# Optimization experiments

Hardware: AMD Instinct MI355X
Metric: run time of the kernel (lower is better)

## Reference

```python
import jax, jax.numpy as jnp
import numpy as np

H = 1024   # hidden_size
V = 1024   # output_size
B = 64     # batch
L = 512    # seq_len


def setup_inputs() -> dict:
    key = jax.random.key(0)
    ks = jax.random.split(key, 14)
    n = jax.random.normal
    s = jnp.float32(0.02)
    return {
        "encoder_output": n(ks[0], (L, B, H), jnp.float32),
        "hidden": n(ks[1], (B, H), jnp.float32),
        "decoder_output": n(ks[2], (B, H), jnp.float32),
        "Wa": n(ks[3], (H, 2 * H), jnp.float32) * s,
        "ba": n(ks[4], (H,), jnp.float32) * s,
        "v": n(ks[5], (H,), jnp.float32) * s,
        "W_ih": n(ks[6], (3 * H, 2 * H), jnp.float32) * s,
        "b_ih": n(ks[7], (3 * H,), jnp.float32) * s,
        "W_hh": n(ks[8], (3 * H, H), jnp.float32) * s,
        "b_hh": n(ks[9], (3 * H,), jnp.float32) * s,
        "Wo": n(ks[10], (H, 3 * H), jnp.float32) * s,
        "bo": n(ks[11], (H,), jnp.float32) * s,
        "Wf": n(ks[12], (V, H), jnp.float32) * s,
        "bf": n(ks[13], (V,), jnp.float32) * s,
    }


def reference(encoder_output, hidden, decoder_output, Wa, ba, v,
              W_ih, b_ih, W_hh, b_hh, Wo, bo, Wf, bf):
    Lx, Bx, Hx = encoder_output.shape
    # energy[b,l] = v . (Wa @ cat(hidden[b], enc[l,b]) + ba)
    # split Wa into hidden-part and encoder-part; fold v into each (linearity)
    Wa_h, Wa_e = Wa[:, :Hx], Wa[:, Hx:]
    vh = Wa_h.T @ v            # (H,)
    ve = Wa_e.T @ v            # (H,)
    vb = ba @ v                # scalar
    # encoder contribution to energies is constant across decode steps
    enc_score = jnp.einsum('lbh,h->bl', encoder_output, ve)  # (B, L)

    def gru_cell(x, h):
        # torch.nn.GRUCell math, gate order [r, z, n]
        gi = x @ W_ih.T + b_ih
        gh = h @ W_hh.T + b_hh
        i_r, i_z, i_n = jnp.split(gi, 3, axis=1)
        h_r, h_z, h_n = jnp.split(gh, 3, axis=1)
        r = jax.nn.sigmoid(i_r + h_r)
        z = jax.nn.sigmoid(i_z + h_z)
        n_g = jnp.tanh(i_n + r * h_n)
        return (1.0 - z) * n_g + z * h

    def step(carry, _):
        h, dec = carry
        energy = (h @ vh + vb)[:, None] + enc_score          # (B, L)
        a = jax.nn.softmax(energy, axis=1)                   # softmax over seq
        ctx = jnp.einsum('bl,lbh->bh', a, encoder_output)    # (B, H)
        h_new = gru_cell(jnp.concatenate([dec, ctx], axis=1), h)
        dec_new = jax.nn.softmax(
            jnp.concatenate([h_new, dec, ctx], axis=1) @ Wo.T + bo, axis=1)
        out = jax.nn.softmax(dec_new @ Wf.T + bf, axis=1)    # (B, V)
        return (h_new, dec_new), out

    _, outs = jax.lax.scan(step, (hidden, decoder_output), None, length=Lx)
    return outs  # (L, B, V)
```

## Files before the change

### kernel.cpp

```cpp
#include <hip/hip_runtime.h>
#include <hip/hip_bf16.h>


#define HH 1024
#define BB 64
#define LL 512
#define VV 1024

typedef short bf16x8 __attribute__((ext_vector_type(8)));
typedef float f32x4 __attribute__((ext_vector_type(4)));

__device__ __forceinline__ short f2bf(float x) {
  union { float f; unsigned u; } a; a.f = x;
  unsigned r = (a.u + 0x7FFF + ((a.u >> 16) & 1)) >> 16;
  return (short)r;
}

__device__ __forceinline__ float fsig(float x) {
  return 1.0f / (1.0f + __expf(-x));
}
__device__ __forceinline__ float ftanh(float x) {
  float ex = __expf(2.0f * x);
  return 1.0f - 2.0f / (ex + 1.0f);
}

__device__ __forceinline__ unsigned long long ld64c(const void* p) {
  return __hip_atomic_load((const unsigned long long*)p, __ATOMIC_RELAXED, __HIP_MEMORY_SCOPE_AGENT);
}
__device__ __forceinline__ unsigned ld32c(const void* p) {
  return __hip_atomic_load((const unsigned*)p, __ATOMIC_RELAXED, __HIP_MEMORY_SCOPE_AGENT);
}
__device__ __forceinline__ void st32c(void* p, unsigned v) {
  __hip_atomic_store((unsigned*)p, v, __ATOMIC_RELAXED, __HIP_MEMORY_SCOPE_AGENT);
}
__device__ __forceinline__ void stfc(float* p, float v) {
  union { float f; unsigned u; } a; a.f = v;
  st32c(p, a.u);
}

static constexpr size_t OFF_VE    = 0;
static constexpr size_t OFF_ES    = 4096;
static constexpr size_t OFF_A     = OFF_ES    + 131072;
static constexpr size_t OFF_CTX   = OFF_A     + 131072;
static constexpr size_t OFF_GICTX = OFF_CTX   + 262144;
static constexpr size_t OFF_OC    = OFF_GICTX + 786432;
static constexpr size_t OFF_FLAGS = OFF_OC    + 262144;
static constexpr size_t OFF_PSUMB = OFF_FLAGS + 32768;
static constexpr size_t OFF_PSUMO = OFF_PSUMB + 16384;
static constexpr size_t OFF_E2    = OFF_PSUMO + 16384;
static constexpr size_t OFF_HB0   = OFF_E2    + 131072;
static constexpr size_t OFF_HB1   = OFF_HB0   + 131072;
static constexpr size_t OFF_PACKW = OFF_HB1   + 131072;


__global__ void K_init(const float* __restrict__ hidden, const float* __restrict__ dec0,
                       short* __restrict__ hb, short* __restrict__ e2,
                       unsigned* __restrict__ flags) {
  int tid = blockIdx.x * 256 + threadIdx.x;
  if (tid < BB * HH) {
    hb[tid] = f2bf(hidden[tid]);
    e2[tid] = f2bf(dec0[tid]);
  }
  if (tid < 8192) flags[tid] = 0u;
}

__global__ void K_ve(const float* __restrict__ Wa, const float* __restrict__ v, float* __restrict__ ve) {
  int i = blockIdx.x * 64 + threadIdx.x;
  float acc = 0.f;
  for (int k = 0; k < HH; ++k) acc += Wa[(size_t)k * 2048 + 1024 + i] * v[k];
  ve[i] = acc;
}

__global__ void K_escore(const float* __restrict__ enc, const float* __restrict__ ve, float* __restrict__ es) {
  int bid = blockIdx.x;
  int lane = threadIdx.x;
  const float* row = enc + (size_t)bid * HH;
  float acc = 0.f;
  #pragma unroll
  for (int i = 0; i < 16; ++i) { int k = lane + 64 * i; acc += row[k] * ve[k]; }
  for (int m = 1; m < 64; m <<= 1) acc += __shfl_xor(acc, m);
  if (lane == 0) { int l = bid >> 6, b = bid & 63; es[b * LL + l] = acc; }
}

__global__ void K_asm(const float* __restrict__ es, float* __restrict__ a) {
  __shared__ float red[256];
  int b = blockIdx.x, tid = threadIdx.x;
  float e0 = es[b * LL + tid], e1 = es[b * LL + 256 + tid];
  red[tid] = fmaxf(e0, e1);
  __syncthreads();
  for (int s = 128; s > 0; s >>= 1) { if (tid < s) red[tid] = fmaxf(red[tid], red[tid + s]); __syncthreads(); }
  float M = red[0];
  __syncthreads();
  float x0 = expf(e0 - M), x1 = expf(e1 - M);
  red[tid] = x0 + x1;
  __syncthreads();
  for (int s = 128; s > 0; s >>= 1) { if (tid < s) red[tid] += red[tid + s]; __syncthreads(); }
  float S = red[0];
  a[b * LL + tid] = x0 / S;
  a[b * LL + 256 + tid] = x1 / S;
}

__global__ void K_ctx(const float* __restrict__ enc, const float* __restrict__ a, float* __restrict__ ctx) {
  int b = blockIdx.x >> 3, hc = blockIdx.x & 7;
  int h = hc * 128 + threadIdx.x;
  float acc = 0.f;
  for (int l = 0; l < LL; ++l) acc += a[b * LL + l] * enc[(size_t)(l * BB + b) * HH + h];
  ctx[b * HH + h] = acc;
}

__global__ void K_gictx(const float* __restrict__ ctx, const float* __restrict__ W_ih, const float* __restrict__ b_ih,
                        const float* __restrict__ Wo, const float* __restrict__ bo,
                        float* __restrict__ gictx, float* __restrict__ oc) {
  int c = blockIdx.x;
  int b = threadIdx.x;
  float acc = 0.f;
  if (c < 3072) {
    for (int k = 0; k < HH; ++k) acc += ctx[b * HH + k] * W_ih[(size_t)c * 2048 + 1024 + k];
    gictx[b * 3072 + c] = acc + b_ih[c];
  } else {
    int c2 = c - 3072;
    for (int k = 0; k < HH; ++k) acc += ctx[b * HH + k] * Wo[(size_t)c2 * 3072 + 2048 + k];
    oc[b * HH + c2] = acc + bo[c2];
  }
}

__global__ void K_pack(const float* __restrict__ W_ih, const float* __restrict__ W_hh,
                       const float* __restrict__ Wo, const float* __restrict__ Wf, short* __restrict__ packW) {
  int tid = blockIdx.x * 64 + threadIdx.x;
  int lane = tid & 63;
  int ks = (tid >> 6) & 31;
  int tile = (tid >> 11) % 9;
  int cg = tid / (9 * 32 * 64);
  int n = lane & 15;
  int k0 = ks * 32 + (lane >> 4) * 8;
  int row = cg * 16 + n;
  const float* src;
  size_t base;
  switch (tile) {
    case 0: base = (size_t)row * 2048;               src = W_ih; break;
    case 1: base = (size_t)(1024 + row) * 2048;      src = W_ih; break;
    case 2: base = (size_t)(2048 + row) * 2048;      src = W_ih; break;
    case 3: base = (size_t)row * 3072 + 1024;        src = Wo;   break;
    case 4: base = (size_t)row * 1024;               src = W_hh; break;
    case 5: base = (size_t)(1024 + row) * 1024;      src = W_hh; break;
    case 6: base = (size_t)(2048 + row) * 1024;      src = W_hh; break;
    case 7: base = (size_t)row * 1024;               src = Wf;   break;
    default: base = (size_t)row * 3072;              src = Wo;   break;
  }
  bf16x8 vv;
  #pragma unroll
  for (int j = 0; j < 8; ++j) vv[j] = f2bf(src[base + k0 + j]);
  ((bf16x8*)packW)[tid] = vv;
}


#define STAGE_SLICE(dst, srcbase)                                              \
  do {                                                                         \
    unsigned long long tv_[16];                                                \
    _Pragma("unroll")                                                          \
    for (int i_ = 0; i_ < 8; ++i_) {                                           \
      int off_ = (wave << 12) + (i_ << 9) + (lane << 3);                       \
      tv_[2 * i_]     = ld64c((srcbase) + off_);                               \
      tv_[2 * i_ + 1] = ld64c((srcbase) + off_ + 4);                           \
    }                                                                          \
    _Pragma("unroll")                                                          \
    for (int i_ = 0; i_ < 8; ++i_) {                                           \
      int off_ = (wave << 12) + (i_ << 9) + (lane << 3);                       \
      int r_ = off_ >> 10;                                                     \
      int bc_ = (off_ & 1023) << 1;                                            \
      int sw_ = bc_ ^ ((r_ & 7) << 4);                                         \
      union { unsigned long long u[2]; bf16x8 v; } x_;                         \
      x_.u[0] = tv_[2 * i_]; x_.u[1] = tv_[2 * i_ + 1];                        \
      *(bf16x8*)&(dst)[(r_ << 10) + (sw_ >> 1)] = x_.v;                        \
    }                                                                          \
  } while (0)

#define LFRAG(buf, ks) \
  (*(const bf16x8*)&(buf)[((llo) << 10) + (((((ks) * 64) + (lhi << 4)) ^ ((llo & 7) << 4)) >> 1)])

__global__ __launch_bounds__(256, 1) void K_step(
    const bf16x8* __restrict__ packW,
    short* __restrict__ e2, short* __restrict__ hb,
    const float* __restrict__ hidden,
    float* __restrict__ psumB, float* __restrict__ psumO,
    const float* __restrict__ gictx, const float* __restrict__ ocbuf,
    const float* __restrict__ b_hh, const float* __restrict__ bfv,
    float* __restrict__ outp, unsigned* __restrict__ flags) {
  const int wg = blockIdx.x;
  const int rg = wg & 3;
  const int cg = wg >> 2;
  const int tid = threadIdx.x;
  const int wave = tid >> 6;
  const int lane = tid & 63;
  const int lhi = lane >> 4;
  const int llo = lane & 15;

  __shared__ short se2[16 * 1024];
  __shared__ short sh[16 * 1024];
  __shared__ float lds_g[6][16][17];
  __shared__ float lds_p[5][16][17];
  __shared__ float lds_rs[16];

  const int wbase = cg * (9 * 32 * 64) + lane;
  const int t0 = wave * 2, t1 = wave * 2 + 1;

  bf16x8 wA0[32], wA1[32], wB8[8];
  #pragma unroll
  for (int ks = 0; ks < 32; ++ks) {
    wA0[ks] = packW[wbase + (t0 * 32 + ks) * 64];
    wA1[ks] = packW[wbase + (t1 * 32 + ks) * 64];
  }
  #pragma unroll
  for (int i = 0; i < 8; ++i) wB8[i] = packW[wbase + (8 * 32 + wave * 8 + i) * 64];
  #pragma unroll
  for (int ks = 0; ks < 32; ++ks) {
    asm volatile("" : "+v"(wA0[ks]));
    asm volatile("" : "+v"(wA1[ks]));
  }
  #pragma unroll
  for (int i = 0; i < 8; ++i) asm volatile("" : "+v"(wB8[i]));

  const int row = tid >> 4, col = tid & 15;
  const int b_ = rg * 16 + row, j = cg * 16 + col;
  const float c_gr  = gictx[b_ * 3072 + j]        + b_hh[j];
  const float c_gz  = gictx[b_ * 3072 + 1024 + j] + b_hh[1024 + j];
  const float c_gn  = gictx[b_ * 3072 + 2048 + j];
  const float c_ghn = b_hh[2048 + j];
  const float c_oc  = ocbuf[b_ * HH + j];
  float h_reg = hidden[b_ * HH + j];
  const float c_bf  = bfv[cg * 16 + llo];

  unsigned* myflags = flags + rg * (64 * 32);
  const short* e2slice = e2 + rg * 16384;
  short*       hslice  = hb + rg * 16384;

  STAGE_SLICE(sh, hslice);

  for (int t = 0; t <= LL; ++t) {
    unsigned long long pc[8];
    if (wave == 0 && t >= 1) {
      const float* pp = psumB + rg * 1024 + llo * 64 + lhi * 16;
      #pragma unroll
      for (int i = 0; i < 8; ++i) pc[i] = ld64c(pp + i * 2);
    }
    STAGE_SLICE(se2, e2slice);
    __syncthreads();

    if (wave == 0) {
      float total = 1.0f;
      if (t >= 1) {
        float s = 0.f;
        #pragma unroll
        for (int i = 0; i < 8; ++i) {
          union { unsigned long long u; float f[2]; } c; c.u = pc[i];
          s += c.f[0] + c.f[1];
        }
        s += __shfl_xor(s, 16);
        s += __shfl_xor(s, 32);
        total = s;
      }
      if (lane < 16) lds_rs[lane] = 1.0f / total;
    }

    const short* A0 = (wave < 2) ? se2 : sh;
    f32x4 acc0 = {0.f, 0.f, 0.f, 0.f}, acc1 = {0.f, 0.f, 0.f, 0.f};
    #pragma unroll
    for (int ks = 0; ks < 32; ++ks) {
      bf16x8 af0 = LFRAG(A0, ks);
      bf16x8 af1 = (wave == 3) ? LFRAG(se2, ks) : af0;
      acc0 = __builtin_amdgcn_mfma_f32_16x16x32_bf16(af0, wA0[ks], acc0, 0, 0, 0);
      acc1 = __builtin_amdgcn_mfma_f32_16x16x32_bf16(af1, wA1[ks], acc1, 0, 0, 0);
    }

    f32x4 savedA2;
    if (wave == 0) {
      #pragma unroll
      for (int r = 0; r < 4; ++r) { lds_g[0][lhi*4+r][llo] = acc0[r]; lds_g[1][lhi*4+r][llo] = acc1[r]; }
    } else if (wave == 1) {
      #pragma unroll
      for (int r = 0; r < 4; ++r) { lds_g[2][lhi*4+r][llo] = acc0[r]; savedA2[r] = acc1[r]; }
    } else if (wave == 2) {
      #pragma unroll
      for (int r = 0; r < 4; ++r) { lds_g[3][lhi*4+r][llo] = acc0[r]; lds_g[4][lhi*4+r][llo] = acc1[r]; }
    } else {
      #pragma unroll
      for (int r = 0; r < 4; ++r) lds_g[5][lhi*4+r][llo] = acc0[r];
    }
    __syncthreads();

    f32x4 eo = {0.f, 0.f, 0.f, 0.f};
    if (wave == 3 && t >= 1) {
      #pragma unroll
      for (int r = 0; r < 4; ++r) eo[r] = __expf(acc1[r] * lds_rs[lhi*4+r] + c_bf);
      #pragma unroll
      for (int r = 0; r < 4; ++r) {
        float v_ = eo[r];
        v_ += __shfl_xor(v_, 1, 16); v_ += __shfl_xor(v_, 2, 16);
        v_ += __shfl_xor(v_, 4, 16); v_ += __shfl_xor(v_, 8, 16);
        if (llo == 0) stfc(psumO + rg * 1024 + (lhi*4+r) * 64 + cg, v_);
      }
    }

    {
      float rsr = lds_rs[row];
      float gr  = lds_g[0][row][col] * rsr + lds_g[3][row][col] + c_gr;
      float gz  = lds_g[1][row][col] * rsr + lds_g[4][row][col] + c_gz;
      float gin = lds_g[2][row][col] * rsr + c_gn;
      float ghn = lds_g[5][row][col] + c_ghn;
      float rr = fsig(gr);
      float zz = fsig(gz);
      float nn = ftanh(gin + rr * ghn);
      float hnew = (1.0f - zz) * nn + zz * h_reg;
      h_reg = hnew;
      unsigned short hv = (unsigned short)f2bf(hnew);
      int other = __shfl_xor((int)hv, 1);
      if ((col & 1) == 0) {
        unsigned pk = (unsigned)hv | ((unsigned)(unsigned short)other << 16);
        st32c(hb + b_ * HH + (j & ~1), pk);
      }
    }

    {
      unsigned ep = 2u * (unsigned)t + 1u;
      __syncthreads();
      if (tid == 0) st32c(myflags + cg * 32, ep);
      if (wave == 0) {
        unsigned f;
        do { f = ld32c(myflags + lane * 32); } while (__any(f < ep));
      }
      __syncthreads();
    }

    if (t < LL) {
      STAGE_SLICE(sh, hslice);
      __syncthreads();
      f32x4 accB = {0.f, 0.f, 0.f, 0.f};
      #pragma unroll
      for (int i = 0; i < 8; ++i) {
        int ks = wave * 8 + i;
        bf16x8 af = LFRAG(sh, ks);
        accB = __builtin_amdgcn_mfma_f32_16x16x32_bf16(af, wB8[i], accB, 0, 0, 0);
      }
      #pragma unroll
      for (int r = 0; r < 4; ++r) lds_p[wave][lhi*4+r][llo] = accB[r];
      if (wave == 1) {
        #pragma unroll
        for (int r = 0; r < 4; ++r) lds_p[4][lhi*4+r][llo] = savedA2[r];
      }
      __syncthreads();
      {
        float rsr = lds_rs[row];
        float l2 = lds_p[0][row][col] + lds_p[1][row][col] + lds_p[2][row][col] + lds_p[3][row][col]
                 + lds_p[4][row][col] * rsr + c_oc;
        float ev = __expf(l2);
        unsigned short eb = (unsigned short)f2bf(ev);
        int other = __shfl_xor((int)eb, 1);
        if ((col & 1) == 0) {
          unsigned pk = (unsigned)eb | ((unsigned)(unsigned short)other << 16);
          st32c(e2 + b_ * HH + (j & ~1), pk);
        }
        float sv = ev;
        sv += __shfl_xor(sv, 1, 16); sv += __shfl_xor(sv, 2, 16);
        sv += __shfl_xor(sv, 4, 16); sv += __shfl_xor(sv, 8, 16);
        if (col == 0) stfc(psumB + rg * 1024 + row * 64 + cg, sv);
      }

      {
        unsigned ep = 2u * (unsigned)t + 2u;
        __syncthreads();
        if (tid == 0) st32c(myflags + cg * 32, ep);
        if (t >= 1 && wave == 3) {
          #pragma unroll
          for (int r = 0; r < 4; ++r) {
            int prow = lhi * 4 + r;
            const float* pp = psumO + rg * 1024 + prow * 64 + llo * 4;
            union { unsigned long long u; float f[2]; } c0, c1;
            c0.u = ld64c(pp); c1.u = ld64c(pp + 2);
            float s = c0.f[0] + c0.f[1] + c1.f[0] + c1.f[1];
            s += __shfl_xor(s, 1, 16); s += __shfl_xor(s, 2, 16);
            s += __shfl_xor(s, 4, 16); s += __shfl_xor(s, 8, 16);
            int b2 = rg * 16 + prow;
            outp[(size_t)(t - 1) * BB * VV + (size_t)b2 * VV + cg * 16 + llo] = eo[r] / s;
          }
        }
        if (wave == 0) {
          unsigned f;
          do { f = ld32c(myflags + lane * 32); } while (__any(f < ep));
        }
        __syncthreads();
      }
    } else {
      if (wave == 3) {
        #pragma unroll
        for (int r = 0; r < 4; ++r) {
          int prow = lhi * 4 + r;
          const float* pp = psumO + rg * 1024 + prow * 64 + llo * 4;
          union { unsigned long long u; float f[2]; } c0, c1;
          c0.u = ld64c(pp); c1.u = ld64c(pp + 2);
          float s = c0.f[0] + c0.f[1] + c1.f[0] + c1.f[1];
          s += __shfl_xor(s, 1, 16); s += __shfl_xor(s, 2, 16);
          s += __shfl_xor(s, 4, 16); s += __shfl_xor(s, 8, 16);
          int b2 = rg * 16 + prow;
          outp[(size_t)(t - 1) * BB * VV + (size_t)b2 * VV + cg * 16 + llo] = eo[r] / s;
        }
      }
    }
  }
}


extern "C" void kernel_launch(void* const* d_in, const int* in_sizes, int n_in,
                              void* d_out, int out_size, void* d_ws, size_t ws_size,
                              hipStream_t stream) {
  (void)in_sizes; (void)n_in; (void)out_size; (void)ws_size;
  const float* enc    = (const float*)d_in[0];
  const float* hidden = (const float*)d_in[1];
  const float* dec0   = (const float*)d_in[2];
  const float* Wa     = (const float*)d_in[3];
  const float* v      = (const float*)d_in[5];
  const float* W_ih   = (const float*)d_in[6];
  const float* b_ih   = (const float*)d_in[7];
  const float* W_hh   = (const float*)d_in[8];
  const float* b_hh   = (const float*)d_in[9];
  const float* Wo     = (const float*)d_in[10];
  const float* bo     = (const float*)d_in[11];
  const float* Wf     = (const float*)d_in[12];
  const float* bfv    = (const float*)d_in[13];

  char* ws = (char*)d_ws;
  float* ve    = (float*)(ws + OFF_VE);
  float* es    = (float*)(ws + OFF_ES);
  float* attn  = (float*)(ws + OFF_A);
  float* ctx   = (float*)(ws + OFF_CTX);
  float* gictx = (float*)(ws + OFF_GICTX);
  float* oc    = (float*)(ws + OFF_OC);
  unsigned* flags = (unsigned*)(ws + OFF_FLAGS);
  float* psumB = (float*)(ws + OFF_PSUMB);
  float* psumO = (float*)(ws + OFF_PSUMO);
  short* e2    = (short*)(ws + OFF_E2);
  short* hb    = (short*)(ws + OFF_HB0);
  short* packW = (short*)(ws + OFF_PACKW);

  hipLaunchKernelGGL(K_init, dim3(256), dim3(256), 0, stream, hidden, dec0, hb, e2, flags);
  hipLaunchKernelGGL(K_ve, dim3(16), dim3(64), 0, stream, Wa, v, ve);
  hipLaunchKernelGGL(K_escore, dim3(LL * BB), dim3(64), 0, stream, enc, ve, es);
  hipLaunchKernelGGL(K_asm, dim3(BB), dim3(256), 0, stream, es, attn);
  hipLaunchKernelGGL(K_ctx, dim3(512), dim3(128), 0, stream, enc, attn, ctx);
  hipLaunchKernelGGL(K_gictx, dim3(4096), dim3(64), 0, stream, ctx, W_ih, b_ih, Wo, bo, gictx, oc);
  hipLaunchKernelGGL(K_pack, dim3(64 * 9 * 32), dim3(64), 0, stream, W_ih, W_hh, Wo, Wf, packW);
  hipLaunchKernelGGL(K_step, dim3(256), dim3(256), 0, stream,
                     (const bf16x8*)packW, e2, hb, hidden, psumB, psumO,
                     gictx, oc, b_hh, bfv, (float*)d_out, flags);
}
```

Before: 5.316 ms.

## Replace per-block flag polling with counter barriers and plain vector loads

Swaps the per-workgroup epoch-flag barrier, where each block polls 64 flags, for a single atomic counter per row group. Arrivals use release fence plus fetch_add, and waiters spin with s_sleep followed by an acquire fence. Shared data (psum, h, e2) is now exchanged with ordinary vectorized loads and stores instead of relaxed atomic 64-bit and 32-bit accesses, relying on the fences for visibility. This aims to cut polling traffic and let the compiler emit wider global loads, but it adds atomic contention on one counter and depends on the fences being correct for cache coherence.

Result: slower. 10.07 ms (+89.3%).

```diff
diff --git a/kernel.cpp b/kernel.cpp
--- a/kernel.cpp
+++ b/kernel.cpp
@@ -22,20 +22,6 @@
 __device__ __forceinline__ float ftanh(float x) {
   float ex = __expf(2.0f * x);
   return 1.0f - 2.0f / (ex + 1.0f);
-}
-
-__device__ __forceinline__ unsigned long long ld64c(const void* p) {
-  return __hip_atomic_load((const unsigned long long*)p, __ATOMIC_RELAXED, __HIP_MEMORY_SCOPE_AGENT);
-}
-__device__ __forceinline__ unsigned ld32c(const void* p) {
-  return __hip_atomic_load((const unsigned*)p, __ATOMIC_RELAXED, __HIP_MEMORY_SCOPE_AGENT);
-}
-__device__ __forceinline__ void st32c(void* p, unsigned v) {
-  __hip_atomic_store((unsigned*)p, v, __ATOMIC_RELAXED, __HIP_MEMORY_SCOPE_AGENT);
-}
-__device__ __forceinline__ void stfc(float* p, float v) {
-  union { float f; unsigned u; } a; a.f = v;
-  st32c(p, a.u);
 }
 
 static constexpr size_t OFF_VE    = 0;
@@ -44,8 +30,8 @@
 static constexpr size_t OFF_CTX   = OFF_A     + 131072;
 static constexpr size_t OFF_GICTX = OFF_CTX   + 262144;
 static constexpr size_t OFF_OC    = OFF_GICTX + 786432;
-static constexpr size_t OFF_FLAGS = OFF_OC    + 262144;
-static constexpr size_t OFF_PSUMB = OFF_FLAGS + 32768;
+static constexpr size_t OFF_CTR   = OFF_OC    + 262144;
+static constexpr size_t OFF_PSUMB = OFF_CTR   + 4096;
 static constexpr size_t OFF_PSUMO = OFF_PSUMB + 16384;
 static constexpr size_t OFF_E2    = OFF_PSUMO + 16384;
 static constexpr size_t OFF_HB0   = OFF_E2    + 131072;
@@ -55,13 +41,13 @@
 
 __global__ void K_init(const float* __restrict__ hidden, const float* __restrict__ dec0,
                        short* __restrict__ hb, short* __restrict__ e2,
-                       unsigned* __restrict__ flags) {
+                       unsigned* __restrict__ ctrs) {
   int tid = blockIdx.x * 256 + threadIdx.x;
   if (tid < BB * HH) {
     hb[tid] = f2bf(hidden[tid]);
     e2[tid] = f2bf(dec0[tid]);
   }
-  if (tid < 8192) flags[tid] = 0u;
+  if (tid < 1024) ctrs[tid] = 0u;
 }
 
 __global__ void K_ve(const float* __restrict__ Wa, const float* __restrict__ v, float* __restrict__ ve) {
@@ -156,12 +142,11 @@
 
 #define STAGE_SLICE(dst, srcbase)                                              \
   do {                                                                         \
-    unsigned long long tv_[16];                                                \
+    bf16x8 tv_[8];                                                             \
     _Pragma("unroll")                                                          \
     for (int i_ = 0; i_ < 8; ++i_) {                                           \
       int off_ = (wave << 12) + (i_ << 9) + (lane << 3);                       \
-      tv_[2 * i_]     = ld64c((srcbase) + off_);                               \
-      tv_[2 * i_ + 1] = ld64c((srcbase) + off_ + 4);                           \
+      tv_[i_] = *(const bf16x8*)((srcbase) + off_);                            \
     }                                                                          \
     _Pragma("unroll")                                                          \
     for (int i_ = 0; i_ < 8; ++i_) {                                           \
@@ -169,9 +154,7 @@
       int r_ = off_ >> 10;                                                     \
       int bc_ = (off_ & 1023) << 1;                                            \
       int sw_ = bc_ ^ ((r_ & 7) << 4);                                         \
-      union { unsigned long long u[2]; bf16x8 v; } x_;                         \
-      x_.u[0] = tv_[2 * i_]; x_.u[1] = tv_[2 * i_ + 1];                        \
-      *(bf16x8*)&(dst)[(r_ << 10) + (sw_ >> 1)] = x_.v;                        \
+      *(bf16x8*)&(dst)[(r_ << 10) + (sw_ >> 1)] = tv_[i_];                     \
     }                                                                          \
   } while (0)
 
@@ -180,12 +163,12 @@
 
 __global__ __launch_bounds__(256, 1) void K_step(
     const bf16x8* __restrict__ packW,
-    short* __restrict__ e2, short* __restrict__ hb,
+    short* e2, short* hb,
     const float* __restrict__ hidden,
-    float* __restrict__ psumB, float* __restrict__ psumO,
+    float* psumB, float* psumO,
     const float* __restrict__ gictx, const float* __restrict__ ocbuf,
     const float* __restrict__ b_hh, const float* __restrict__ bfv,
-    float* __restrict__ outp, unsigned* __restrict__ flags) {
+    float* __restrict__ outp, unsigned* ctrs) {
   const int wg = blockIdx.x;
   const int rg = wg & 3;
   const int cg = wg >> 2;
@@ -230,18 +213,19 @@
   float h_reg = hidden[b_ * HH + j];
   const float c_bf  = bfv[cg * 16 + llo];
 
-  unsigned* myflags = flags + rg * (64 * 32);
+  unsigned* ctr1 = ctrs + rg * 64;
+  unsigned* ctr2 = ctrs + rg * 64 + 32;
   const short* e2slice = e2 + rg * 16384;
   short*       hslice  = hb + rg * 16384;
 
   STAGE_SLICE(sh, hslice);
 
   for (int t = 0; t <= LL; ++t) {
-    unsigned long long pc[8];
+    f32x4 pc0, pc1, pc2, pc3;
     if (wave == 0 && t >= 1) {
       const float* pp = psumB + rg * 1024 + llo * 64 + lhi * 16;
-      #pragma unroll
-      for (int i = 0; i < 8; ++i) pc[i] = ld64c(pp + i * 2);
+      pc0 = *(const f32x4*)pp;       pc1 = *(const f32x4*)(pp + 4);
+      pc2 = *(const f32x4*)(pp + 8); pc3 = *(const f32x4*)(pp + 12);
     }
     STAGE_SLICE(se2, e2slice);
     __syncthreads();
@@ -249,12 +233,8 @@
     if (wave == 0) {
       float total = 1.0f;
       if (t >= 1) {
-        float s = 0.f;
-        #pragma unroll
-        for (int i = 0; i < 8; ++i) {
-          union { unsigned long long u; float f[2]; } c; c.u = pc[i];
-          s += c.f[0] + c.f[1];
-        }
+        float s = (pc0[0] + pc0[1] + pc0[2] + pc0[3]) + (pc1[0] + pc1[1] + pc1[2] + pc1[3])
+                + (pc2[0] + pc2[1] + pc2[2] + pc2[3]) + (pc3[0] + pc3[1] + pc3[2] + pc3[3]);
         s += __shfl_xor(s, 16);
         s += __shfl_xor(s, 32);
         total = s;
@@ -297,7 +277,7 @@
         float v_ = eo[r];
         v_ += __shfl_xor(v_, 1, 16); v_ += __shfl_xor(v_, 2, 16);
         v_ += __shfl_xor(v_, 4, 16); v_ += __shfl_xor(v_, 8, 16);
-        if (llo == 0) stfc(psumO + rg * 1024 + (lhi*4+r) * 64 + cg, v_);
+        if (llo == 0) psumO[rg * 1024 + (lhi*4+r) * 64 + cg] = v_;
       }
     }
 
@@ -316,17 +296,25 @@
       int other = __shfl_xor((int)hv, 1);
       if ((col & 1) == 0) {
         unsigned pk = (unsigned)hv | ((unsigned)(unsigned short)other << 16);
-        st32c(hb + b_ * HH + (j & ~1), pk);
+        *(unsigned*)(hb + b_ * HH + (j & ~1)) = pk;
       }
     }
 
     {
-      unsigned ep = 2u * (unsigned)t + 1u;
+      unsigned tgt = 64u * (unsigned)(t + 1);
       __syncthreads();
-      if (tid == 0) st32c(myflags + cg * 32, ep);
+      if (tid == 0) {
+        __builtin_amdgcn_fence(__ATOMIC_RELEASE, "agent");
+        __hip_atomic_fetch_add(ctr1, 1u, __ATOMIC_RELAXED, __HIP_MEMORY_SCOPE_AGENT);
+      }
       if (wave == 0) {
-        unsigned f;
-        do { f = ld32c(myflags + lane * 32); } while (__any(f < ep));
+        unsigned c_;
+        do {
+          c_ = __hip_atomic_load(ctr1, __ATOMIC_RELAXED, __HIP_MEMORY_SCOPE_AGENT);
+          if (c_ >= tgt) break;
+          __builtin_amdgcn_s_sleep(1);
+        } while (1);
+        __builtin_amdgcn_fence(__ATOMIC_ACQUIRE, "agent");
       }
       __syncthreads();
     }
@@ -357,26 +345,27 @@
         int other = __shfl_xor((int)eb, 1);
         if ((col & 1) == 0) {
           unsigned pk = (unsigned)eb | ((unsigned)(unsigned short)other << 16);
-          st32c(e2 + b_ * HH + (j & ~1), pk);
+          *(unsigned*)(e2 + b_ * HH + (j & ~1)) = pk;
         }
         float sv = ev;
         sv += __shfl_xor(sv, 1, 16); sv += __shfl_xor(sv, 2, 16);
         sv += __shfl_xor(sv, 4, 16); sv += __shfl_xor(sv, 8, 16);
-        if (col == 0) stfc(psumB + rg * 1024 + row * 64 + cg, sv);
+        if (col == 0) psumB[rg * 1024 + row * 64 + cg] = sv;
       }
 
       {
-        unsigned ep = 2u * (unsigned)t + 2u;
+        unsigned tgt = 64u * (unsigned)(t + 1);
         __syncthreads();
-        if (tid == 0) st32c(myflags + cg * 32, ep);
+        if (tid == 0) {
+          __builtin_amdgcn_fence(__ATOMIC_RELEASE, "agent");
+          __hip_atomic_fetch_add(ctr2, 1u, __ATOMIC_RELAXED, __HIP_MEMORY_SCOPE_AGENT);
+        }
         if (t >= 1 && wave == 3) {
           #pragma unroll
           for (int r = 0; r < 4; ++r) {
             int prow = lhi * 4 + r;
-            const float* pp = psumO + rg * 1024 + prow * 64 + llo * 4;
-            union { unsigned long long u; float f[2]; } c0, c1;
-            c0.u = ld64c(pp); c1.u = ld64c(pp + 2);
-            float s = c0.f[0] + c0.f[1] + c1.f[0] + c1.f[1];
+            f32x4 c4 = *(const f32x4*)(psumO + rg * 1024 + prow * 64 + llo * 4);
+            float s = c4[0] + c4[1] + c4[2] + c4[3];
             s += __shfl_xor(s, 1, 16); s += __shfl_xor(s, 2, 16);
             s += __shfl_xor(s, 4, 16); s += __shfl_xor(s, 8, 16);
             int b2 = rg * 16 + prow;
@@ -384,8 +373,13 @@
           }
         }
         if (wave == 0) {
-          unsigned f;
-          do { f = ld32c(myflags + lane * 32); } while (__any(f < ep));
+          unsigned c_;
+          do {
+            c_ = __hip_atomic_load(ctr2, __ATOMIC_RELAXED, __HIP_MEMORY_SCOPE_AGENT);
+            if (c_ >= tgt) break;
+            __builtin_amdgcn_s_sleep(1);
+          } while (1);
+          __builtin_amdgcn_fence(__ATOMIC_ACQUIRE, "agent");
         }
         __syncthreads();
       }
@@ -394,10 +388,8 @@
         #pragma unroll
         for (int r = 0; r < 4; ++r) {
           int prow = lhi * 4 + r;
-          const float* pp = psumO + rg * 1024 + prow * 64 + llo * 4;
-          union { unsigned long long u; float f[2]; } c0, c1;
-          c0.u = ld64c(pp); c1.u = ld64c(pp + 2);
-          float s = c0.f[0] + c0.f[1] + c1.f[0] + c1.f[1];
+          f32x4 c4 = *(const f32x4*)(psumO + rg * 1024 + prow * 64 + llo * 4);
+          float s = c4[0] + c4[1] + c4[2] + c4[3];
           s += __shfl_xor(s, 1, 16); s += __shfl_xor(s, 2, 16);
           s += __shfl_xor(s, 4, 16); s += __shfl_xor(s, 8, 16);
           int b2 = rg * 16 + prow;
@@ -434,14 +426,14 @@
   float* ctx   = (float*)(ws + OFF_CTX);
   float* gictx = (float*)(ws + OFF_GICTX);
   float* oc    = (float*)(ws + OFF_OC);
-  unsigned* flags = (unsigned*)(ws + OFF_FLAGS);
+  unsigned* ctrs = (unsigned*)(ws + OFF_CTR);
   float* psumB = (float*)(ws + OFF_PSUMB);
   float* psumO = (float*)(ws + OFF_PSUMO);
   short* e2    = (short*)(ws + OFF_E2);
   short* hb    = (short*)(ws + OFF_HB0);
   short* packW = (short*)(ws + OFF_PACKW);
 
-  hipLaunchKernelGGL(K_init, dim3(256), dim3(256), 0, stream, hidden, dec0, hb, e2, flags);
+  hipLaunchKernelGGL(K_init, dim3(256), dim3(256), 0, stream, hidden, dec0, hb, e2, ctrs);
   hipLaunchKernelGGL(K_ve, dim3(16), dim3(64), 0, stream, Wa, v, ve);
   hipLaunchKernelGGL(K_escore, dim3(LL * BB), dim3(64), 0, stream, enc, ve, es);
   hipLaunchKernelGGL(K_asm, dim3(BB), dim3(256), 0, stream, es, attn);
@@ -450,5 +442,5 @@
   hipLaunchKernelGGL(K_pack, dim3(64 * 9 * 32), dim3(64), 0, stream, W_ih, W_hh, Wo, Wf, packW);
   hipLaunchKernelGGL(K_step, dim3(256), dim3(256), 0, stream,
                      (const bf16x8*)packW, e2, hb, hidden, psumB, psumO,
-                     gictx, oc, b_hh, bfv, (float*)d_out, flags);
-}
+                     gictx, oc, b_hh, bfv, (float*)d_out, ctrs);
+}
```

## Double-buffer e2/psumB and replace grid barriers with per-block flag polling

Applied to the files above, without the earlier changes.

The persistent step kernel now double-buffers the e2 activations and the psumB partial sums by step parity, so the second grid-wide barrier per step can be removed. Each wave waits only on the 16 producer workgroups whose column block it stages (POLL16), and that wait is folded into the staging load instead of a separate wave-0 spin plus __syncthreads. Staging uses inline-asm dwordx4 loads, the psumO loads are issued earlier, and output stores become nontemporal. The intent is to cut the synchronization latency on every one of the 512 sequential steps, at the cost of more subtle memory-ordering assumptions in the flag protocol.

New measurement: 6.518 ms. 22.6% more time.

```diff
diff --git a/kernel.cpp b/kernel.cpp
--- a/kernel.cpp
+++ b/kernel.cpp
@@ -46,20 +46,20 @@
 static constexpr size_t OFF_OC    = OFF_GICTX + 786432;
 static constexpr size_t OFF_FLAGS = OFF_OC    + 262144;
 static constexpr size_t OFF_PSUMB = OFF_FLAGS + 32768;
-static constexpr size_t OFF_PSUMO = OFF_PSUMB + 16384;
-static constexpr size_t OFF_E2    = OFF_PSUMO + 16384;
-static constexpr size_t OFF_HB0   = OFF_E2    + 131072;
-static constexpr size_t OFF_HB1   = OFF_HB0   + 131072;
-static constexpr size_t OFF_PACKW = OFF_HB1   + 131072;
+static constexpr size_t OFF_PSUMO = OFF_PSUMB + 32768;
+static constexpr size_t OFF_E2A   = OFF_PSUMO + 16384;
+static constexpr size_t OFF_HB    = OFF_E2A   + 131072;
+static constexpr size_t OFF_E2B   = OFF_HB    + 131072;
+static constexpr size_t OFF_PACKW = OFF_E2B   + 131072;
 
 
 __global__ void K_init(const float* __restrict__ hidden, const float* __restrict__ dec0,
-                       short* __restrict__ hb, short* __restrict__ e2,
+                       short* __restrict__ hb, short* __restrict__ e2a,
                        unsigned* __restrict__ flags) {
   int tid = blockIdx.x * 256 + threadIdx.x;
   if (tid < BB * HH) {
     hb[tid] = f2bf(hidden[tid]);
-    e2[tid] = f2bf(dec0[tid]);
+    e2a[tid] = f2bf(dec0[tid]);
   }
   if (tid < 8192) flags[tid] = 0u;
 }
@@ -154,33 +154,63 @@
 }
 
 
-#define STAGE_SLICE(dst, srcbase)                                              \
+#define STAGE_BLOCK(dst, srcbase, blk)                                         \
   do {                                                                         \
-    unsigned long long tv_[16];                                                \
+    const int r_ = lane >> 2;                                                  \
+    const int co_ = ((blk) << 8) + ((lane & 3) << 6);       \
+    const short* p_ = (srcbase) + (r_ << 10) + co_;                            \
+    f32x4 t0_, t1_, t2_, t3_, t4_, t5_, t6_, t7_;                              \
+    asm volatile(                                                              \
+      "global_load_dwordx4 %0, %8, off sc0 sc1\n\t"                            \
+      "global_load_dwordx4 %1, %8, off offset:16 sc0 sc1\n\t"                  \
+      "global_load_dwordx4 %2, %8, off offset:32 sc0 sc1\n\t"                  \
+      "global_load_dwordx4 %3, %8, off offset:48 sc0 sc1\n\t"                  \
+      "global_load_dwordx4 %4, %8, off offset:64 sc0 sc1\n\t"                  \
+      "global_load_dwordx4 %5, %8, off offset:80 sc0 sc1\n\t"                  \
+      "global_load_dwordx4 %6, %8, off offset:96 sc0 sc1\n\t"                  \
+      "global_load_dwordx4 %7, %8, off offset:112 sc0 sc1\n\t"                 \
+      "s_waitcnt vmcnt(0)"                                                     \
+      : "=&v"(t0_), "=&v"(t1_), "=&v"(t2_), "=&v"(t3_),                        \
+        "=&v"(t4_), "=&v"(t5_), "=&v"(t6_), "=&v"(t7_)                         \
+      : "v"(p_)                                                                \
+      : "memory");                                                             \
+    f32x4 tv_[8] = {t0_, t1_, t2_, t3_, t4_, t5_, t6_, t7_};                   \
     _Pragma("unroll")                                                          \
     for (int i_ = 0; i_ < 8; ++i_) {                                           \
-      int off_ = (wave << 12) + (i_ << 9) + (lane << 3);                       \
-      tv_[2 * i_]     = ld64c((srcbase) + off_);                               \
-      tv_[2 * i_ + 1] = ld64c((srcbase) + off_ + 4);                           \
+      int bc_ = (co_ + (i_ << 3)) << 1;                                        \
+      int sw_ = bc_ ^ ((r_ & 7) << 4);                                         \
+      *(f32x4*)&(dst)[(r_ << 10) + (sw_ >> 1)] = tv_[i_];                      \
     }                                                                          \
-    _Pragma("unroll")                                                          \
-    for (int i_ = 0; i_ < 8; ++i_) {                                           \
-      int off_ = (wave << 12) + (i_ << 9) + (lane << 3);                       \
-      int r_ = off_ >> 10;                                                     \
-      int bc_ = (off_ & 1023) << 1;                                            \
-      int sw_ = bc_ ^ ((r_ & 7) << 4);                                         \
-      union { unsigned long long u[2]; bf16x8 v; } x_;                         \
-      x_.u[0] = tv_[2 * i_]; x_.u[1] = tv_[2 * i_ + 1];                        \
-      *(bf16x8*)&(dst)[(r_ << 10) + (sw_ >> 1)] = x_.v;                        \
+    __builtin_amdgcn_sched_barrier(0);                                         \
+  } while (0)
+
+#define POLL16(flg, blk, ep)                                                   \
+  do {                                                                         \
+    unsigned f_;                                                               \
+    for (;;) {                                                                 \
+      f_ = ld32c((flg) + ((blk) * 16 + (lane & 15)) * 32);                     \
+      if (!__any(f_ < (unsigned)(ep))) break;                                  \
+      __builtin_amdgcn_s_sleep(1);                                             \
     }                                                                          \
   } while (0)
 
+#define POLL64(flg, ep)                                                        \
+  do {                                                                         \
+    unsigned f_;                                                               \
+    for (;;) {                                                                 \
+      f_ = ld32c((flg) + lane * 32);                                           \
+      if (!__any(f_ < (unsigned)(ep))) break;                                  \
+      __builtin_amdgcn_s_sleep(1);                                             \
+    }                                                                          \
+  } while (0)
+
 #define LFRAG(buf, ks) \
   (*(const bf16x8*)&(buf)[((llo) << 10) + (((((ks) * 64) + (lhi << 4)) ^ ((llo & 7) << 4)) >> 1)])
 
 __global__ __launch_bounds__(256, 1) void K_step(
     const bf16x8* __restrict__ packW,
-    short* __restrict__ e2, short* __restrict__ hb,
+    short* __restrict__ e2a, short* __restrict__ e2b,
+    short* __restrict__ hb,
     const float* __restrict__ hidden,
     float* __restrict__ psumB, float* __restrict__ psumO,
     const float* __restrict__ gictx, const float* __restrict__ ocbuf,
@@ -194,6 +224,7 @@
   const int lane = tid & 63;
   const int lhi = lane >> 4;
   const int llo = lane & 15;
+  const int blk = (wave + cg) & 3;
 
   __shared__ short se2[16 * 1024];
   __shared__ short sh[16 * 1024];
@@ -231,19 +262,30 @@
   const float c_bf  = bfv[cg * 16 + llo];
 
   unsigned* myflags = flags + rg * (64 * 32);
-  const short* e2slice = e2 + rg * 16384;
-  short*       hslice  = hb + rg * 16384;
-
-  STAGE_SLICE(sh, hslice);
+  short* hslice = hb + rg * 16384;
+
+  STAGE_BLOCK(sh, hslice, blk);
 
   for (int t = 0; t <= LL; ++t) {
+    const int par = t & 1;
+    const short* ebr = (par ? e2b : e2a) + rg * 16384;
+    short* ebw = par ? e2a : e2b;
+    const float* PBr = psumB + par * 4096 + rg * 1024;
+    float* PBw = psumB + (par ^ 1) * 4096 + rg * 1024;
+
     unsigned long long pc[8];
-    if (wave == 0 && t >= 1) {
-      const float* pp = psumB + rg * 1024 + llo * 64 + lhi * 16;
-      #pragma unroll
-      for (int i = 0; i < 8; ++i) pc[i] = ld64c(pp + i * 2);
-    }
-    STAGE_SLICE(se2, e2slice);
+    if (wave == 0) {
+      POLL64(myflags, 2u * (unsigned)t);
+      if (t >= 1) {
+        const float* pp = PBr + llo * 64 + lhi * 16;
+        #pragma unroll
+        for (int i = 0; i < 8; ++i) pc[i] = ld64c(pp + i * 2);
+      }
+      STAGE_BLOCK(se2, ebr, blk);
+    } else {
+      POLL16(myflags, blk, 2u * (unsigned)t);
+      STAGE_BLOCK(se2, ebr, blk);
+    }
     __syncthreads();
 
     if (wave == 0) {
@@ -320,20 +362,24 @@
       }
     }
 
-    {
-      unsigned ep = 2u * (unsigned)t + 1u;
+    __syncthreads();
+    if (tid == 0) st32c(myflags + cg * 32, 2u * (unsigned)t + 1u);
+
+    if (t < LL) {
+      POLL16(myflags, blk, 2u * (unsigned)t + 1u);
+      STAGE_BLOCK(sh, hslice, blk);
       __syncthreads();
-      if (tid == 0) st32c(myflags + cg * 32, ep);
-      if (wave == 0) {
-        unsigned f;
-        do { f = ld32c(myflags + lane * 32); } while (__any(f < ep));
-      }
-      __syncthreads();
-    }
-
-    if (t < LL) {
-      STAGE_SLICE(sh, hslice);
-      __syncthreads();
+
+      union { unsigned long long u; float f[2]; } g0[4], g1[4];
+      if (wave == 3 && t >= 1) {
+        #pragma unroll
+        for (int r = 0; r < 4; ++r) {
+          const float* pp = psumO + rg * 1024 + (lhi * 4 + r) * 64 + llo * 4;
+          g0[r].u = ld64c(pp);
+          g1[r].u = ld64c(pp + 2);
+        }
+      }
+
       f32x4 accB = {0.f, 0.f, 0.f, 0.f};
       #pragma unroll
       for (int i = 0; i < 8; ++i) {
@@ -357,50 +403,40 @@
         int other = __shfl_xor((int)eb, 1);
         if ((col & 1) == 0) {
           unsigned pk = (unsigned)eb | ((unsigned)(unsigned short)other << 16);
-          st32c(e2 + b_ * HH + (j & ~1), pk);
+          st32c(ebw + b_ * HH + (j & ~1), pk);
         }
         float sv = ev;
         sv += __shfl_xor(sv, 1, 16); sv += __shfl_xor(sv, 2, 16);
         sv += __shfl_xor(sv, 4, 16); sv += __shfl_xor(sv, 8, 16);
-        if (col == 0) stfc(psumB + rg * 1024 + row * 64 + cg, sv);
-      }
-
-      {
-        unsigned ep = 2u * (unsigned)t + 2u;
-        __syncthreads();
-        if (tid == 0) st32c(myflags + cg * 32, ep);
-        if (t >= 1 && wave == 3) {
-          #pragma unroll
-          for (int r = 0; r < 4; ++r) {
-            int prow = lhi * 4 + r;
-            const float* pp = psumO + rg * 1024 + prow * 64 + llo * 4;
-            union { unsigned long long u; float f[2]; } c0, c1;
-            c0.u = ld64c(pp); c1.u = ld64c(pp + 2);
-            float s = c0.f[0] + c0.f[1] + c1.f[0] + c1.f[1];
-            s += __shfl_xor(s, 1, 16); s += __shfl_xor(s, 2, 16);
-            s += __shfl_xor(s, 4, 16); s += __shfl_xor(s, 8, 16);
-            int b2 = rg * 16 + prow;
-            outp[(size_t)(t - 1) * BB * VV + (size_t)b2 * VV + cg * 16 + llo] = eo[r] / s;
-          }
+        if (col == 0) stfc(PBw + row * 64 + cg, sv);
+      }
+
+      if (wave == 3 && t >= 1) {
+        #pragma unroll
+        for (int r = 0; r < 4; ++r) {
+          float s = g0[r].f[0] + g0[r].f[1] + g1[r].f[0] + g1[r].f[1];
+          s += __shfl_xor(s, 1, 16); s += __shfl_xor(s, 2, 16);
+          s += __shfl_xor(s, 4, 16); s += __shfl_xor(s, 8, 16);
+          int b2 = rg * 16 + lhi * 4 + r;
+          __builtin_nontemporal_store(eo[r] / s,
+            &outp[(size_t)(t - 1) * BB * VV + (size_t)b2 * VV + cg * 16 + llo]);
         }
-        if (wave == 0) {
-          unsigned f;
-          do { f = ld32c(myflags + lane * 32); } while (__any(f < ep));
-        }
-        __syncthreads();
-      }
+      }
+
+      __syncthreads();
+      if (tid == 0) st32c(myflags + cg * 32, 2u * (unsigned)t + 2u);
     } else {
       if (wave == 3) {
+        POLL64(myflags, 2u * (unsigned)t + 1u);
         #pragma unroll
         for (int r = 0; r < 4; ++r) {
-          int prow = lhi * 4 + r;
-          const float* pp = psumO + rg * 1024 + prow * 64 + llo * 4;
+          const float* pp = psumO + rg * 1024 + (lhi * 4 + r) * 64 + llo * 4;
           union { unsigned long long u; float f[2]; } c0, c1;
           c0.u = ld64c(pp); c1.u = ld64c(pp + 2);
           float s = c0.f[0] + c0.f[1] + c1.f[0] + c1.f[1];
           s += __shfl_xor(s, 1, 16); s += __shfl_xor(s, 2, 16);
           s += __shfl_xor(s, 4, 16); s += __shfl_xor(s, 8, 16);
-          int b2 = rg * 16 + prow;
+          int b2 = rg * 16 + lhi * 4 + r;
           outp[(size_t)(t - 1) * BB * VV + (size_t)b2 * VV + cg * 16 + llo] = eo[r] / s;
         }
       }
@@ -437,11 +473,12 @@
   unsigned* flags = (unsigned*)(ws + OFF_FLAGS);
   float* psumB = (float*)(ws + OFF_PSUMB);
   float* psumO = (float*)(ws + OFF_PSUMO);
-  short* e2    = (short*)(ws + OFF_E2);
-  short* hb    = (short*)(ws + OFF_HB0);
+  short* e2a   = (short*)(ws + OFF_E2A);
+  short* e2b   = (short*)(ws + OFF_E2B);
+  short* hb    = (short*)(ws + OFF_HB);
   short* packW = (short*)(ws + OFF_PACKW);
 
-  hipLaunchKernelGGL(K_init, dim3(256), dim3(256), 0, stream, hidden, dec0, hb, e2, flags);
+  hipLaunchKernelGGL(K_init, dim3(256), dim3(256), 0, stream, hidden, dec0, hb, e2a, flags);
   hipLaunchKernelGGL(K_ve, dim3(16), dim3(64), 0, stream, Wa, v, ve);
   hipLaunchKernelGGL(K_escore, dim3(LL * BB), dim3(64), 0, stream, enc, ve, es);
   hipLaunchKernelGGL(K_asm, dim3(BB), dim3(256), 0, stream, es, attn);
@@ -449,6 +486,6 @@
   hipLaunchKernelGGL(K_gictx, dim3(4096), dim3(64), 0, stream, ctx, W_ih, b_ih, Wo, bo, gictx, oc);
   hipLaunchKernelGGL(K_pack, dim3(64 * 9 * 32), dim3(64), 0, stream, W_ih, W_hh, Wo, Wf, packW);
   hipLaunchKernelGGL(K_step, dim3(256), dim3(256), 0, stream,
-                     (const bf16x8*)packW, e2, hb, hidden, psumB, psumO,
+                     (const bf16x8*)packW, e2a, e2b, hb, hidden, psumB, psumO,
                      gictx, oc, b_hh, bfv, (float*)d_out, flags);
 }
```
